# Kernel tuning notes

Hardware: AMD Instinct MI355X
Metric: run time of the kernel (lower is better)

## Reference

```python
import jax, jax.numpy as jnp
import numpy as np
from functools import partial

H = 2048   # image height
W = 2048   # image width
FC_IN = 1024
FC_OUT = 10


def setup_inputs() -> dict:
    key = jax.random.key(0)
    ks = jax.random.split(key, 7)
    x = jax.random.normal(ks[0], (1, H, W), dtype=jnp.float32)
    # Conv2d(1,1,1): scalar weight + bias
    w_in = jax.random.normal(ks[1], (1, 1, 1, 1), dtype=jnp.float32)
    b_in = jax.random.normal(ks[2], (1,), dtype=jnp.float32) * 0.1
    # Conv1d(1,1,2,padding=1): 2-tap kernel + bias
    w_state = jax.random.normal(ks[3], (1, 1, 2), dtype=jnp.float32) * 0.5
    b_state = jax.random.normal(ks[4], (1,), dtype=jnp.float32) * 0.1
    # Linear(1024, 10)
    fc_w = jax.random.normal(ks[5], (FC_OUT, FC_IN), dtype=jnp.float32) * (1.0 / np.sqrt(FC_IN))
    fc_b = jax.random.normal(ks[6], (FC_OUT,), dtype=jnp.float32) * 0.1
    return {"x": x, "w_in": w_in, "b_in": b_in, "w_state": w_state,
            "b_state": b_state, "fc_w": fc_w, "fc_b": fc_b}


def reference(x, w_in, b_in, w_state, b_state, fc_w, fc_b):
    img = x[0]                      # [H, W]
    h_dim, w_dim = img.shape
    w_skew = w_dim + h_dim - 1      # skewed image width

    # --- skew: row r shifted right by r, zero-filled elsewhere ---
    rows = jnp.arange(h_dim)[:, None]          # [H,1]
    cols = jnp.arange(w_dim)[None, :] + rows   # [H,W] destination columns
    skewed = jnp.zeros((h_dim, w_skew), dtype=img.dtype).at[rows, cols].set(img)

    # --- 1x1 input convolution: scalar affine ---
    input_matrix = skewed * w_in[0, 0, 0, 0] + b_in[0]   # [H, Wskew]

    k0 = w_state[0, 0, 0]
    k1 = w_state[0, 0, 1]
    bs = b_state[0]

    # --- sequential column scan: h_c = tanh(k0*shift(h) + k1*h + bs + inp_c) ---
    def step(h, inp_col):
        shifted = jnp.concatenate([jnp.zeros((1,), h.dtype), h[:-1]])
        a = jnp.tanh(k0 * shifted + k1 * h + bs + inp_col)
        return a, a

    h0 = jnp.zeros((h_dim,), dtype=img.dtype)
    _, acts = jax.lax.scan(step, h0, input_matrix.T)     # acts: [Wskew, H]

    # --- unskew: unskewed[r, c] = acts[r + c, r] ---
    c_idx = jnp.arange(w_dim)[None, :]                   # [1, W]
    unskewed = acts[rows + c_idx, rows]                  # [H, W]

    flat = unskewed.reshape(-1, FC_IN)                   # [H*W/1024, 1024]
    return flat @ fc_w.T + fc_b                          # [H*W/1024, 10]
```

## Files before the change

kernel.cpp:

```cpp
#include <hip/hip_runtime.h>

#define HH 2048
#define WW 2048
#define WSK 4095
#define WSKP 4096
#define BLKS 8
#define NW  4
#define NT  (NW * 64)
#define KCH 32
#define NCH (WSKP / KCH)
#define FC_IN 1024
#define FC_OUT 10
#define NFLAT ((HH * WW) / FC_IN)

__device__ __forceinline__ float tanh_pre(float xs) {
  float e = __builtin_amdgcn_exp2f(xs);
  float r = __builtin_amdgcn_rcpf(e + 1.0f);
  return __builtin_fmaf(-2.0f, r, 1.0f);
}

__device__ __forceinline__ float wave_shr1(float src, float old) {
  int r = __builtin_amdgcn_update_dpp(
      __builtin_bit_cast(int, old), __builtin_bit_cast(int, src),
      0x138 , 0xF, 0xF, false);
  return __builtin_bit_cast(float, r);
}

__global__ __launch_bounds__(256) void skew_kernel(
    const float* __restrict__ img, const float* __restrict__ w_in,
    const float* __restrict__ b_in, const float* __restrict__ b_state,
    float* __restrict__ inp) {
  const float S = 2.88539008177792681472f;
  const float ws = w_in[0] * S;
  const float Cs = (b_in[0] + b_state[0]) * S;
  int gid = blockIdx.x * 256 + threadIdx.x;
  int r = gid & (HH - 1);
  int c = gid >> 11;
  int idx = c - r;
  float v = Cs;
  if ((unsigned)idx < (unsigned)WW) v = fmaf(ws, img[(size_t)r * WW + idx], Cs);
  inp[gid] = v;
}

__global__ __launch_bounds__(NT) void scan_kernel(
    const float* __restrict__ w_state, const float* __restrict__ inp,
    float* __restrict__ acts, unsigned* __restrict__ flags) {
  const int t = threadIdx.x;
  const int wv = t >> 6;
  const int lane = t & 63;
  const int blk = blockIdx.x;
  const int r = blk * NT + t;

  const float S = 2.88539008177792681472f;
  const float k0s = w_state[0] * S;
  const float k1s = w_state[1] * S;

  __shared__ float ring[2][NW][KCH];

  float h = 0.0f;
  const float* colp_in = inp + r;
  float* colp_out = acts + r;

  float pf[KCH];
  #pragma unroll
  for (int d = 0; d < KCH; ++d) pf[d] = colp_in[(size_t)d * HH];

  const unsigned* upflag = flags + (blk - 1) * NCH;
  unsigned* myflag = flags + blk * NCH;
  const float* uprow = acts + (blk * NT - 1);

  for (int e = 0; e < NCH + NW - 1; ++e) {
    const int ch = e - wv;
    if (0 <= ch && ch < NCH) {
      const int c0 = ch * KCH;

      float bvec;
      if (wv == 0) {
        bvec = 0.0f;
        if (blk > 0) {
          const unsigned want = (unsigned)(ch + 1);
          while (__hip_atomic_load(upflag + ch, __ATOMIC_ACQUIRE,
                                   __HIP_MEMORY_SCOPE_AGENT) != want)
            __builtin_amdgcn_s_sleep(1);
          int cl = c0 + lane - 1;
          if (lane < KCH && cl >= 0) bvec = uprow[(size_t)cl * HH];
        }
      } else {
        bvec = ring[(e & 1) ^ 1][wv - 1][lane & (KCH - 1)];
      }
      if (lane == 63) ring[e & 1][wv][0] = h;

      const int cb = (ch + 1 < NCH ? ch + 1 : ch) * KCH;

      #pragma unroll
      for (int cc = 0; cc < KCH; ++cc) {
        float cur = pf[cc];
        pf[cc] = colp_in[(size_t)(cb + cc) * HH];

        float pv = __builtin_bit_cast(float,
            __builtin_amdgcn_readlane(__builtin_bit_cast(int, bvec), cc));
        float prev = wave_shr1(h, pv);

        h = tanh_pre(fmaf(k0s, prev, fmaf(k1s, h, cur)));

        if (lane == 63 && cc + 1 < KCH) ring[e & 1][wv][cc + 1] = h;
        colp_out[(size_t)(c0 + cc) * HH] = h;
      }

      if (wv == NW - 1 && lane == 63)
        __hip_atomic_store(myflag + ch, (unsigned)(ch + 1), __ATOMIC_RELEASE,
                           __HIP_MEMORY_SCOPE_AGENT);
    }
    asm volatile("s_waitcnt lgkmcnt(0)\n\ts_barrier" ::: "memory");
  }
}

__global__ __launch_bounds__(64) void fc_kernel(
    const float* __restrict__ acts, const float* __restrict__ fc_w,
    const float* __restrict__ fc_b, float* __restrict__ out) {
  const int i = blockIdx.x;
  const int lane = threadIdx.x;
  const int r = i >> 1;
  const int base = (i & 1) << 10;

  float acc[FC_OUT];
  #pragma unroll
  for (int j = 0; j < FC_OUT; ++j) acc[j] = 0.0f;

  for (int k = lane; k < FC_IN; k += 64) {
    float v = acts[(size_t)(r + base + k) * HH + r];
    #pragma unroll
    for (int j = 0; j < FC_OUT; ++j)
      acc[j] = fmaf(v, fc_w[j * FC_IN + k], acc[j]);
  }

  #pragma unroll
  for (int j = 0; j < FC_OUT; ++j) {
    #pragma unroll
    for (int off = 32; off > 0; off >>= 1)
      acc[j] += __shfl_down(acc[j], off);
  }

  if (lane == 0) {
    #pragma unroll
    for (int j = 0; j < FC_OUT; ++j)
      out[i * FC_OUT + j] = acc[j] + fc_b[j];
  }
}

extern "C" void kernel_launch(void* const* d_in, const int* in_sizes, int n_in,
                              void* d_out, int out_size, void* d_ws, size_t ws_size,
                              hipStream_t stream) {
  const float* x       = (const float*)d_in[0];
  const float* w_in    = (const float*)d_in[1];
  const float* b_in    = (const float*)d_in[2];
  const float* w_state = (const float*)d_in[3];
  const float* b_state = (const float*)d_in[4];
  const float* fc_w    = (const float*)d_in[5];
  const float* fc_b    = (const float*)d_in[6];
  float* out = (float*)d_out;
  float* buf = (float*)d_ws;

  unsigned* flags = (unsigned*)d_out;

  skew_kernel<<<(WSKP * HH) / 256, 256, 0, stream>>>(x, w_in, b_in, b_state, buf);
  scan_kernel<<<BLKS, NT, 0, stream>>>(w_state, buf, buf, flags);
  fc_kernel<<<NFLAT, 64, 0, stream>>>(buf, fc_w, fc_b, out);
}
```

Baseline: 554.2 us.

## Prefetch upstream boundary chunk ahead via contiguous boundary buffer in scan

The last wave of each scan block now also writes its boundary row into a contiguous side buffer placed in the output region. The first wave of the next block waits for the flag of chunk ch+1 and loads it while chunk ch is being computed, instead of waiting and doing a strided load right before use. Input columns for the next chunk are also loaded in one batch into a second register array rather than interleaved with the recurrence. The aim is to take the flag-wait and boundary-load latency off the serial critical path. The cost is a one-chunk-deeper dependency between blocks, which lengthens pipeline fill, plus higher register use.

```diff
diff --git a/kernel.cpp b/kernel.cpp
--- a/kernel.cpp
+++ b/kernel.cpp
@@ -44,7 +44,8 @@
 
 __global__ __launch_bounds__(NT) void scan_kernel(
     const float* __restrict__ w_state, const float* __restrict__ inp,
-    float* __restrict__ acts, unsigned* __restrict__ flags) {
+    float* __restrict__ acts, float* __restrict__ bnd,
+    unsigned* __restrict__ flags) {
   const int t = threadIdx.x;
   const int wv = t >> 6;
   const int lane = t & 63;
@@ -61,55 +62,70 @@
   const float* colp_in = inp + r;
   float* colp_out = acts + r;
 
-  float pf[KCH];
+  float cur[KCH], nxt[KCH];
   #pragma unroll
-  for (int d = 0; d < KCH; ++d) pf[d] = colp_in[(size_t)d * HH];
+  for (int d = 0; d < KCH; ++d) cur[d] = colp_in[(size_t)d * HH];
 
   const unsigned* upflag = flags + (blk - 1) * NCH;
   unsigned* myflag = flags + blk * NCH;
-  const float* uprow = acts + (blk * NT - 1);
+  const float* upbnd = bnd + (size_t)(blk - 1) * WSKP;
+  float* mybnd = bnd + (size_t)blk * WSKP;
+
+  float bcur = 0.0f, bnext = 0.0f;
+  if (wv == 0 && blk > 0) {
+    while (__hip_atomic_load(upflag + 0, __ATOMIC_RELAXED,
+                             __HIP_MEMORY_SCOPE_AGENT) != 1u)
+      __builtin_amdgcn_s_sleep(1);
+    __builtin_amdgcn_fence(__ATOMIC_ACQUIRE, "agent");
+    if (lane < KCH && lane >= 1) bcur = upbnd[lane - 1];
+  }
 
   for (int e = 0; e < NCH + NW - 1; ++e) {
     const int ch = e - wv;
     if (0 <= ch && ch < NCH) {
       const int c0 = ch * KCH;
 
+      if (wv == 0 && blk > 0 && ch + 1 < NCH) {
+        const unsigned want = (unsigned)(ch + 2);
+        while (__hip_atomic_load(upflag + (ch + 1), __ATOMIC_RELAXED,
+                                 __HIP_MEMORY_SCOPE_AGENT) != want)
+          __builtin_amdgcn_s_sleep(1);
+        __builtin_amdgcn_fence(__ATOMIC_ACQUIRE, "agent");
+        bnext = 0.0f;
+        if (lane < KCH) bnext = upbnd[c0 + KCH + lane - 1];
+      }
+
       float bvec;
-      if (wv == 0) {
-        bvec = 0.0f;
-        if (blk > 0) {
-          const unsigned want = (unsigned)(ch + 1);
-          while (__hip_atomic_load(upflag + ch, __ATOMIC_ACQUIRE,
-                                   __HIP_MEMORY_SCOPE_AGENT) != want)
-            __builtin_amdgcn_s_sleep(1);
-          int cl = c0 + lane - 1;
-          if (lane < KCH && cl >= 0) bvec = uprow[(size_t)cl * HH];
-        }
-      } else {
-        bvec = ring[(e & 1) ^ 1][wv - 1][lane & (KCH - 1)];
-      }
+      if (wv == 0) bvec = bcur;
+      else bvec = ring[(e & 1) ^ 1][wv - 1][lane & (KCH - 1)];
       if (lane == 63) ring[e & 1][wv][0] = h;
 
       const int cb = (ch + 1 < NCH ? ch + 1 : ch) * KCH;
+      #pragma unroll
+      for (int cc = 0; cc < KCH; ++cc)
+        nxt[cc] = colp_in[(size_t)(cb + cc) * HH];
 
       #pragma unroll
       for (int cc = 0; cc < KCH; ++cc) {
-        float cur = pf[cc];
-        pf[cc] = colp_in[(size_t)(cb + cc) * HH];
-
         float pv = __builtin_bit_cast(float,
             __builtin_amdgcn_readlane(__builtin_bit_cast(int, bvec), cc));
         float prev = wave_shr1(h, pv);
 
-        h = tanh_pre(fmaf(k0s, prev, fmaf(k1s, h, cur)));
+        h = tanh_pre(fmaf(k0s, prev, fmaf(k1s, h, cur[cc])));
 
         if (lane == 63 && cc + 1 < KCH) ring[e & 1][wv][cc + 1] = h;
+        if (wv == NW - 1 && blk < BLKS - 1 && lane == 63)
+          mybnd[c0 + cc] = h;
         colp_out[(size_t)(c0 + cc) * HH] = h;
       }
 
-      if (wv == NW - 1 && lane == 63)
+      if (wv == NW - 1 && blk < BLKS - 1 && lane == 63)
         __hip_atomic_store(myflag + ch, (unsigned)(ch + 1), __ATOMIC_RELEASE,
                            __HIP_MEMORY_SCOPE_AGENT);
+      if (wv == 0) bcur = bnext;
+
+      #pragma unroll
+      for (int cc = 0; cc < KCH; ++cc) cur[cc] = nxt[cc];
     }
     asm volatile("s_waitcnt lgkmcnt(0)\n\ts_barrier" ::: "memory");
   }
@@ -162,8 +178,9 @@
   float* buf = (float*)d_ws;
 
   unsigned* flags = (unsigned*)d_out;
+  float* bnd = out + 1024;
 
   skew_kernel<<<(WSKP * HH) / 256, 256, 0, stream>>>(x, w_in, b_in, b_state, buf);
-  scan_kernel<<<BLKS, NT, 0, stream>>>(w_state, buf, buf, flags);
+  scan_kernel<<<BLKS, NT, 0, stream>>>(w_state, buf, buf, bnd, flags);
   fc_kernel<<<NFLAT, 64, 0, stream>>>(buf, fc_w, fc_b, out);
 }
```

Result: slower. 615.1 us (+11.0%).
